# Kernel optimization log

Measured on AMD Instinct MI355X. Metric: run time of the kernel, lower is better.

## Reference

```python
import jax, jax.numpy as jnp
import numpy as np

N_NODES = 100_000
N_EDGES = 1_600_000
IN_F = 256
HID = 256
OUT_F = 256
BN_EPS = 1e-5


def make_quaternion_mul(kernel):
    # kernel: [d, 4m] -> hamilton: [4d, 4m]
    dim = kernel.shape[1] // 4
    r, i, j, k = jnp.split(kernel, 4, axis=1)
    r2 = jnp.concatenate([r, -i, -j, -k], axis=0)
    i2 = jnp.concatenate([i, r, -k, j], axis=0)
    j2 = jnp.concatenate([j, k, r, -i], axis=0)
    k2 = jnp.concatenate([k, -j, i, r], axis=0)
    return jnp.concatenate([r2, i2, j2, k2], axis=1)


def setup_inputs() -> dict:
    key = jax.random.key(0)
    ks = jax.random.split(key, 6)
    x = jax.random.normal(ks[0], (N_NODES, IN_F), dtype=jnp.float32)
    rows = jax.random.randint(ks[1], (N_EDGES,), 0, N_NODES, dtype=jnp.int32)
    cols = jax.random.randint(ks[2], (N_EDGES,), 0, N_NODES, dtype=jnp.int32)
    edge_vals = jax.random.uniform(ks[3], (N_EDGES,), dtype=jnp.float32)
    stdv1 = np.sqrt(6.0 / (IN_F // 4 + HID))
    weight1 = jax.random.uniform(ks[4], (IN_F // 4, HID), dtype=jnp.float32,
                                 minval=-stdv1, maxval=stdv1)
    stdv2 = np.sqrt(6.0 / (HID // 4 + OUT_F))
    weight2 = jax.random.uniform(ks[5], (HID // 4, OUT_F), dtype=jnp.float32,
                                 minval=-stdv2, maxval=stdv2)
    gamma = jnp.ones((HID,), dtype=jnp.float32)
    beta = jnp.zeros((HID,), dtype=jnp.float32)
    return {"x": x, "rows": rows, "cols": cols, "edge_vals": edge_vals,
            "weight1": weight1, "weight2": weight2, "gamma": gamma, "beta": beta}


def reference(x, rows, cols, edge_vals, weight1, weight2, gamma, beta):
    hamilton1 = make_quaternion_mul(weight1)  # [IN_F, HID]
    hamilton2 = make_quaternion_mul(weight2)  # [HID, OUT_F]
    # spmm: new_x[r] = sum_e adj[r,c]*x[c] over edges (r=rows, c=cols)
    gathered = edge_vals[:, None] * x[cols]               # [E, IN_F]
    new_x = jax.ops.segment_sum(gathered, rows, num_segments=N_NODES)
    out1 = new_x @ hamilton1                              # [N, HID]
    # BatchNorm1d (training mode): biased batch stats over nodes
    mean = jnp.mean(out1, axis=0)
    var = jnp.mean(jnp.square(out1 - mean), axis=0)
    out1 = (out1 - mean) * jax.lax.rsqrt(var + BN_EPS) * gamma + beta
    out1 = jnp.tanh(out1)
    return out1 @ hamilton2                               # [N, OUT_F]
```

## Files before the change

kernel.cpp:

```cpp
#include <hip/hip_runtime.h>
#include <hip/hip_bf16.h>
#include <math.h>


#define FDIM 256
#define NREP 32
#define CH 2048

typedef __attribute__((ext_vector_type(8))) short bf16x8;
typedef __attribute__((ext_vector_type(4))) float f32x4;

static __device__ inline short f2bf(float x) {
    __hip_bfloat16 h = __float2bfloat16(x);
    return *reinterpret_cast<short*>(&h);
}
static __device__ inline float bf2f(unsigned short u) {
    union { unsigned int i; float f; } c;
    c.i = ((unsigned int)u) << 16;
    return c.f;
}
static __device__ inline float bflo(unsigned int u) {
    union { unsigned int i; float f; } c;
    c.i = u << 16;
    return c.f;
}
static __device__ inline float bfhi(unsigned int u) {
    union { unsigned int i; float f; } c;
    c.i = u & 0xFFFF0000u;
    return c.f;
}
static __device__ inline float fast_tanh(float x) {
    float e = __expf(2.f * x);
    return 1.f - 2.f * __builtin_amdgcn_rcpf(e + 1.f);
}

static __device__ void build_hfrag(const float* __restrict__ w, ushort* __restrict__ hf,
                                   int t) {
    const int   comp_t[16] = {0,1,2,3,  1,0,3,2,  2,3,0,1,  3,2,1,0};
    const float sign_t[16] = {1,1,1,1, -1,1,1,-1, -1,-1,1,1, -1,1,-1,1};
    int f = t >> 6, lane = t & 63;
    int tile = f >> 3, kk = f & 7;
    int col = tile * 16 + (lane & 15);
    int b = col >> 6, q = col & 63;
    ushort o[8];
#pragma unroll
    for (int j = 0; j < 8; ++j) {
        int k = kk * 32 + ((lane >> 4) << 3) + j;
        int a = k >> 6, p = k & 63;
        int ab = a * 4 + b;
        float v = sign_t[ab] * w[p * 256 + comp_t[ab] * 64 + q];
        o[j] = (ushort)f2bf(v);
    }
    *(ushort4*)(hf + (size_t)t * 8)     = make_ushort4(o[0], o[1], o[2], o[3]);
    *(ushort4*)(hf + (size_t)t * 8 + 4) = make_ushort4(o[4], o[5], o[6], o[7]);
}

__global__ void k_init(const float* __restrict__ w1, const float* __restrict__ w2,
                       ushort* __restrict__ h1f, ushort* __restrict__ h2f,
                       float* __restrict__ statsR) {
    int b = blockIdx.x;
    if (b < 32) {
        build_hfrag(w1, h1f, b * 256 + threadIdx.x);
    } else if (b < 64) {
        build_hfrag(w2, h2f, (b - 32) * 256 + threadIdx.x);
    } else {
        int slot = (b - 64) * 256 + threadIdx.x;
        *(float4*)(statsR + slot * 4) = make_float4(0.f, 0.f, 0.f, 0.f);
    }
}

__global__ __launch_bounds__(256) void k_p1(const int* __restrict__ rows,
                                            int* __restrict__ CM,
                                            int E, int nchunk, int NB) {
    __shared__ int lc[256];
    int t = threadIdx.x, c = blockIdx.x;
    lc[t] = 0;
    __syncthreads();
#pragma unroll
    for (int i = 0; i < 8; ++i) {
        int e = c * CH + i * 256 + t;
        if (e < E) atomicAdd(&lc[rows[e] >> 9], 1);
    }
    __syncthreads();
    if (t < NB) CM[t * nchunk + c] = lc[t];
}

__global__ __launch_bounds__(256) void k_p2(const int* __restrict__ CM,
                                            int* __restrict__ PO,
                                            int* __restrict__ BT, int nchunk) {
    __shared__ int ts[256];
    int t = threadIdx.x, b = blockIdx.x;
    int base = b * nchunk;
    int lex[4], s = 0;
#pragma unroll
    for (int i = 0; i < 4; ++i) {
        int c = t * 4 + i;
        int v = (c < nchunk) ? CM[base + c] : 0;
        lex[i] = s;
        s += v;
    }
    ts[t] = s;
    __syncthreads();
    for (int off = 1; off < 256; off <<= 1) {
        int v = (t >= off) ? ts[t - off] : 0;
        __syncthreads();
        ts[t] += v;
        __syncthreads();
    }
    int excl = ts[t] - s;
#pragma unroll
    for (int i = 0; i < 4; ++i) {
        int c = t * 4 + i;
        if (c < nchunk) PO[base + c] = excl + lex[i];
    }
    if (t == 255) BT[b] = ts[255];
}

__global__ __launch_bounds__(256) void k_p3(const int* __restrict__ rows,
                                            const int* __restrict__ cols,
                                            const float* __restrict__ vals,
                                            const int* __restrict__ PO,
                                            const int* __restrict__ BT,
                                            uint2* __restrict__ tmp2,
                                            int E, int nchunk, int NB) {
    __shared__ int sBB[256];
    __shared__ int sPO[256];
    __shared__ int sLC[256];
    int t = threadIdx.x, c = blockIdx.x;
    int own = (t < NB) ? BT[t] : 0;
    sBB[t] = own;
    sPO[t] = (t < NB) ? PO[t * nchunk + c] : 0;
    sLC[t] = 0;
    __syncthreads();
    for (int off = 1; off < 256; off <<= 1) {
        int v = (t >= off) ? sBB[t - off] : 0;
        __syncthreads();
        sBB[t] += v;
        __syncthreads();
    }
    sBB[t] -= own;
    __syncthreads();
#pragma unroll
    for (int i = 0; i < 8; ++i) {
        int e = c * CH + i * 256 + t;
        if (e < E) {
            int r = rows[e];
            int b = r >> 9;
            int rank = atomicAdd(&sLC[b], 1);
            int pos = sBB[b] + sPO[b] + rank;
            int iv = (int)(vals[e] * 32768.0f);
            tmp2[pos] = make_uint2((unsigned int)cols[e] | ((unsigned int)iv << 17),
                                   (unsigned int)r);
        }
    }
}

__global__ __launch_bounds__(1024) void k_p4(const uint2* __restrict__ tmp2,
                                             const int* __restrict__ BT,
                                             unsigned int* __restrict__ ew,
                                             int* __restrict__ offs,
                                             int N, int NB) {
    __shared__ int sBB[256];
    __shared__ int sH[512];
    __shared__ int sO[512];
    __shared__ int sC[512];
    int t = threadIdx.x, b = blockIdx.x;
    int own = 0;
    if (t < 256) {
        own = (t < NB) ? BT[t] : 0;
        sBB[t] = own;
    }
    __syncthreads();
    for (int off = 1; off < 256; off <<= 1) {
        int v = (t < 256 && t >= off) ? sBB[t - off] : 0;
        __syncthreads();
        if (t < 256) sBB[t] += v;
        __syncthreads();
    }
    if (t < 256) sBB[t] -= own;
    if (t < 512) sH[t] = 0;
    __syncthreads();
    const int base = sBB[b];
    const int nE = BT[b];
    const int rbase = b << 9;
    for (int i = t; i < nE; i += 1024)
        atomicAdd(&sH[(int)tmp2[base + i].y - rbase], 1);
    __syncthreads();
    if (t < 512) sO[t] = sH[t];
    __syncthreads();
    for (int off = 1; off < 512; off <<= 1) {
        int v = (t < 512 && t >= off) ? sO[t - off] : 0;
        __syncthreads();
        if (t < 512) sO[t] += v;
        __syncthreads();
    }
    if (t < 512) {
        sO[t] -= sH[t];
        int r = rbase + t;
        if (r <= N) offs[r] = base + sO[t];
        sC[t] = 0;
    }
    __syncthreads();
    for (int i = t; i < nE; i += 1024) {
        uint2 u = tmp2[base + i];
        int lr = (int)u.y - rbase;
        int p = atomicAdd(&sC[lr], 1);
        ew[base + sO[lr] + p] = u.x;
    }
}

__global__ __launch_bounds__(256) void k_gemm1(const float* __restrict__ X,
                                               const ushort* __restrict__ Bf,
                                               ushort* __restrict__ Y, int N) {
    __shared__ ushort lds[16384];
    const int t = threadIdx.x;
    const int w = t >> 6, lane = t & 63;
    const int r0 = blockIdx.x * 128 + w * 32;
    const int kbase = ((lane >> 4) & 3) * 8;
    const int rA[2] = { min(r0 + (lane & 15), N - 1),
                        min(r0 + 16 + (lane & 15), N - 1) };

    bf16x8 af[2][8];
#pragma unroll
    for (int rt = 0; rt < 2; ++rt)
#pragma unroll
        for (int kk = 0; kk < 8; ++kk) {
            const float* p = X + (size_t)rA[rt] * 256 + kk * 32 + kbase;
            float4 v0 = *(const float4*)p;
            float4 v1 = *(const float4*)(p + 4);
            bf16x8 a;
            a[0] = f2bf(v0.x); a[1] = f2bf(v0.y); a[2] = f2bf(v0.z); a[3] = f2bf(v0.w);
            a[4] = f2bf(v1.x); a[5] = f2bf(v1.y); a[6] = f2bf(v1.z); a[7] = f2bf(v1.w);
            af[rt][kk] = a;
        }

    for (int g = 0; g < 4; ++g) {
        {
            const float4* s4 = (const float4*)(Bf + (size_t)g * 16384 + t * 64);
            float4* d4 = (float4*)(lds + t * 64);
#pragma unroll
            for (int i = 0; i < 8; ++i) d4[i] = s4[i];
        }
        __syncthreads();

        f32x4 acc[2][4];
#pragma unroll
        for (int rt = 0; rt < 2; ++rt)
#pragma unroll
            for (int tg = 0; tg < 4; ++tg) acc[rt][tg] = (f32x4){0.f, 0.f, 0.f, 0.f};

#pragma unroll
        for (int tg = 0; tg < 4; ++tg)
#pragma unroll
            for (int kk = 0; kk < 8; ++kk) {
                bf16x8 b = *(const bf16x8*)(lds + ((tg * 8 + kk) * 64 + lane) * 8);
                acc[0][tg] = __builtin_amdgcn_mfma_f32_16x16x32_bf16(af[0][kk], b, acc[0][tg], 0, 0, 0);
                acc[1][tg] = __builtin_amdgcn_mfma_f32_16x16x32_bf16(af[1][kk], b, acc[1][tg], 0, 0, 0);
            }

#pragma unroll
        for (int tg = 0; tg < 4; ++tg) {
            int col = (g * 4 + tg) * 16 + (lane & 15);
#pragma unroll
            for (int rt = 0; rt < 2; ++rt) {
                int rbase = r0 + rt * 16 + ((lane >> 4) & 3) * 4;
#pragma unroll
                for (int j = 0; j < 4; ++j) {
                    int r = rbase + j;
                    if (r < N) Y[(size_t)r * 256 + col] = (ushort)f2bf(acc[rt][tg][j]);
                }
            }
        }
        __syncthreads();
    }
}

__global__ __launch_bounds__(256) void k_spmm(const ushort* __restrict__ Y,
                                              const int* __restrict__ offs,
                                              const unsigned int* __restrict__ ew,
                                              ushort* __restrict__ O,
                                              float* __restrict__ statsR, int n) {
    __shared__ float ls[8][256];
    const int tid = threadIdx.x;
    int wid = (blockIdx.x * blockDim.x + tid) >> 6;
    int w = tid >> 6, lane = tid & 63;
    int l32 = lane & 31;
    int row = wid * 2 + (lane >> 5);
    bool ok = row < n;
    int r = ok ? row : 0;
    int beg = offs[r];
    int cnt = ok ? (offs[r + 1] - beg) : 0;
    int g = (cnt + 7) >> 3;
    const unsigned int* ep = ew + beg;

    float a0 = 0.f, a1 = 0.f, a2 = 0.f, a3 = 0.f;
    float a4 = 0.f, a5 = 0.f, a6 = 0.f, a7 = 0.f;

    for (int gi = 0; gi < g; ++gi) {
        unsigned int wv[8];
#pragma unroll
        for (int i = 0; i < 8; ++i) wv[i] = ep[gi * 8 + i];
        uint4 u[8];
#pragma unroll
        for (int i = 0; i < 8; ++i) {
            int c = (gi * 8 + i < cnt) ? (int)(wv[i] & 0x1FFFFu) : 0;
            u[i] = *(const uint4*)(Y + (size_t)c * 256 + l32 * 8);
        }
#pragma unroll
        for (int i = 0; i < 8; ++i) {
            float v = (gi * 8 + i < cnt) ? (float)(wv[i] >> 17) * (1.0f / 32768.0f) : 0.f;
            a0 = fmaf(v, bflo(u[i].x), a0); a1 = fmaf(v, bfhi(u[i].x), a1);
            a2 = fmaf(v, bflo(u[i].y), a2); a3 = fmaf(v, bfhi(u[i].y), a3);
            a4 = fmaf(v, bflo(u[i].z), a4); a5 = fmaf(v, bfhi(u[i].z), a5);
            a6 = fmaf(v, bflo(u[i].w), a6); a7 = fmaf(v, bfhi(u[i].w), a7);
        }
    }
    if (ok) {
        unsigned int p0 = ((unsigned int)(unsigned short)f2bf(a0)) |
                          (((unsigned int)(unsigned short)f2bf(a1)) << 16);
        unsigned int p1 = ((unsigned int)(unsigned short)f2bf(a2)) |
                          (((unsigned int)(unsigned short)f2bf(a3)) << 16);
        unsigned int p2 = ((unsigned int)(unsigned short)f2bf(a4)) |
                          (((unsigned int)(unsigned short)f2bf(a5)) << 16);
        unsigned int p3 = ((unsigned int)(unsigned short)f2bf(a6)) |
                          (((unsigned int)(unsigned short)f2bf(a7)) << 16);
        *(uint4*)(O + (size_t)r * 512 + l32 * 8) = make_uint4(p0, p1, p2, p3);
    }

    int h2 = w * 2 + (lane >> 5);
    int fb = l32 * 8;
    int rep = blockIdx.x & (NREP - 1);
    *(float4*)&ls[h2][fb]     = make_float4(a0, a1, a2, a3);
    *(float4*)&ls[h2][fb + 4] = make_float4(a4, a5, a6, a7);
    __syncthreads();
    float sv = 0.f;
#pragma unroll
    for (int i = 0; i < 8; ++i) sv += ls[i][tid];
    atomicAdd(&statsR[rep * 256 + tid], sv);
    __syncthreads();
    *(float4*)&ls[h2][fb]     = make_float4(a0 * a0, a1 * a1, a2 * a2, a3 * a3);
    *(float4*)&ls[h2][fb + 4] = make_float4(a4 * a4, a5 * a5, a6 * a6, a7 * a7);
    __syncthreads();
    float qv = 0.f;
#pragma unroll
    for (int i = 0; i < 8; ++i) qv += ls[i][tid];
    atomicAdd(&statsR[NREP * 256 + rep * 256 + tid], qv);
}

__global__ __launch_bounds__(256) void k_gemm2(void* __restrict__ Av,
                                               const ushort* __restrict__ Bf,
                                               const float* __restrict__ statsR,
                                               const float* __restrict__ gamma,
                                               const float* __restrict__ beta, int N) {
    __shared__ ushort lds[16384];
    __shared__ float sscl[256], sshf[256];
    const int t = threadIdx.x;
    const int w = t >> 6, lane = t & 63;
    const int r0 = blockIdx.x * 128 + w * 32;
    const int kbase = ((lane >> 4) & 3) * 8;
    const int rA[2] = { min(r0 + (lane & 15), N - 1),
                        min(r0 + 16 + (lane & 15), N - 1) };

    {
        float s = 0.f, q = 0.f;
#pragma unroll
        for (int i = 0; i < NREP; ++i) {
            s += statsR[i * 256 + t];
            q += statsR[NREP * 256 + i * 256 + t];
        }
        float invn = 1.0f / (float)N;
        float mean = s * invn;
        float var = q * invn - mean * mean;
        float inv = rsqrtf(var + 1e-5f);
        float gg = gamma[t] * inv;
        sscl[t] = gg;
        sshf[t] = beta[t] - mean * gg;
        __syncthreads();
    }

    const ushort* X = (const ushort*)Av;
    bf16x8 af[2][8];
#pragma unroll
    for (int rt = 0; rt < 2; ++rt)
#pragma unroll
        for (int kk = 0; kk < 8; ++kk) {
            const ushort* p = X + (size_t)rA[rt] * 512 + kk * 32 + kbase;
            ushort4 u0 = *(const ushort4*)p;
            ushort4 u1 = *(const ushort4*)(p + 4);
            float4 s0 = *(const float4*)&sscl[kk * 32 + kbase];
            float4 s1 = *(const float4*)&sscl[kk * 32 + kbase + 4];
            float4 h0 = *(const float4*)&sshf[kk * 32 + kbase];
            float4 h1 = *(const float4*)&sshf[kk * 32 + kbase + 4];
            bf16x8 a;
            a[0] = f2bf(fast_tanh(fmaf(bf2f(u0.x), s0.x, h0.x)));
            a[1] = f2bf(fast_tanh(fmaf(bf2f(u0.y), s0.y, h0.y)));
            a[2] = f2bf(fast_tanh(fmaf(bf2f(u0.z), s0.z, h0.z)));
            a[3] = f2bf(fast_tanh(fmaf(bf2f(u0.w), s0.w, h0.w)));
            a[4] = f2bf(fast_tanh(fmaf(bf2f(u1.x), s1.x, h1.x)));
            a[5] = f2bf(fast_tanh(fmaf(bf2f(u1.y), s1.y, h1.y)));
            a[6] = f2bf(fast_tanh(fmaf(bf2f(u1.z), s1.z, h1.z)));
            a[7] = f2bf(fast_tanh(fmaf(bf2f(u1.w), s1.w, h1.w)));
            af[rt][kk] = a;
        }

    float* Cf = (float*)Av;
    for (int g = 0; g < 4; ++g) {
        {
            const float4* s4 = (const float4*)(Bf + (size_t)g * 16384 + t * 64);
            float4* d4 = (float4*)(lds + t * 64);
#pragma unroll
            for (int i = 0; i < 8; ++i) d4[i] = s4[i];
        }
        __syncthreads();

        f32x4 acc[2][4];
#pragma unroll
        for (int rt = 0; rt < 2; ++rt)
#pragma unroll
            for (int tg = 0; tg < 4; ++tg) acc[rt][tg] = (f32x4){0.f, 0.f, 0.f, 0.f};

#pragma unroll
        for (int tg = 0; tg < 4; ++tg)
#pragma unroll
            for (int kk = 0; kk < 8; ++kk) {
                bf16x8 b = *(const bf16x8*)(lds + ((tg * 8 + kk) * 64 + lane) * 8);
                acc[0][tg] = __builtin_amdgcn_mfma_f32_16x16x32_bf16(af[0][kk], b, acc[0][tg], 0, 0, 0);
                acc[1][tg] = __builtin_amdgcn_mfma_f32_16x16x32_bf16(af[1][kk], b, acc[1][tg], 0, 0, 0);
            }

#pragma unroll
        for (int tg = 0; tg < 4; ++tg) {
            int col = (g * 4 + tg) * 16 + (lane & 15);
#pragma unroll
            for (int rt = 0; rt < 2; ++rt) {
                int rbase = r0 + rt * 16 + ((lane >> 4) & 3) * 4;
#pragma unroll
                for (int j = 0; j < 4; ++j) {
                    int r = rbase + j;
                    if (r < N) Cf[(size_t)r * 256 + col] = acc[rt][tg][j];
                }
            }
        }
        __syncthreads();
    }
}

extern "C" void kernel_launch(void* const* d_in, const int* in_sizes, int n_in,
                              void* d_out, int out_size, void* d_ws, size_t ws_size,
                              hipStream_t stream) {
    const float* x     = (const float*)d_in[0];
    const int* rows    = (const int*)d_in[1];
    const int* cols    = (const int*)d_in[2];
    const float* evin  = (const float*)d_in[3];
    const float* w1    = (const float*)d_in[4];
    const float* w2    = (const float*)d_in[5];
    const float* gamma = (const float*)d_in[6];
    const float* beta  = (const float*)d_in[7];
    float* out = (float*)d_out;

    const int N = in_sizes[0] / FDIM;
    const int E = in_sizes[1];
    const int NB = (N + 511) >> 9;
    const int nchunk = (E + CH - 1) / CH;

    char* ws = (char*)d_ws;
    size_t o = 0;
    auto alloc = [&](size_t bytes) -> char* {
        char* p = ws + o;
        o += (bytes + 255) & ~(size_t)255;
        return p;
    };
    ushort* h1f  = (ushort*)alloc(128 * 64 * 8 * 2);
    ushort* h2f  = (ushort*)alloc(128 * 64 * 8 * 2);
    ushort* y    = (ushort*)alloc((size_t)N * 256 * 2);
    float* statsR = (float*)alloc(2 * NREP * 256 * 4);
    int*   CM    = (int*)alloc((size_t)NB * nchunk * 4);
    int*   PO    = (int*)alloc((size_t)NB * nchunk * 4);
    int*   BT    = (int*)alloc(256 * 4);
    uint2* tmp2  = (uint2*)alloc((size_t)E * 8);
    unsigned int* ewp = (unsigned int*)alloc(((size_t)E + 8) * 4);
    int*   offs  = (int*)alloc((size_t)(N + 1) * 4);

    k_init<<<80, 256, 0, stream>>>(w1, w2, h1f, h2f, statsR);
    k_p1<<<nchunk, 256, 0, stream>>>(rows, CM, E, nchunk, NB);
    k_p2<<<NB, 256, 0, stream>>>(CM, PO, BT, nchunk);
    k_p3<<<nchunk, 256, 0, stream>>>(rows, cols, evin, PO, BT, tmp2, E, nchunk, NB);
    k_p4<<<NB, 1024, 0, stream>>>(tmp2, BT, ewp, offs, N, NB);

    int gblk = (N + 127) / 128;
    k_gemm1<<<gblk, 256, 0, stream>>>(x, h1f, y, N);
    k_spmm<<<(N + 7) / 8, 256, 0, stream>>>(y, offs, ewp, (ushort*)out, statsR, N);
    k_gemm2<<<gblk, 256, 0, stream>>>(out, h2f, statsR, gamma, beta, N);
}
```

Baseline: 295.0 us.

## Prefetch GEMM weight tiles into registers and remap SpMM to one row per wave

Both GEMM kernels now load the next weight group into registers while the current group computes, hiding global-load latency behind the MFMA work. The SpMM kernel assigns one full wave per row (4 features per lane, 8-byte loads) instead of a half-wave per row, and software-prefetches the next batch of packed edge words. This doubles the SpMM grid size and the number of stats atomics, adds register pressure in the GEMMs, and enlarges the edge buffer padding to cover the prefetch reads.

After: 353.8 us. 1.2x slower.

```diff
diff --git a/kernel.cpp b/kernel.cpp
--- a/kernel.cpp
+++ b/kernel.cpp
@@ -234,14 +234,24 @@
             af[rt][kk] = a;
         }
 
+    float4 breg[8];
+#pragma unroll
+    for (int i = 0; i < 8; ++i)
+        breg[i] = ((const float4*)(Bf + (size_t)0 * 16384 + t * 64))[i];
+
+#pragma unroll
     for (int g = 0; g < 4; ++g) {
         {
-            const float4* s4 = (const float4*)(Bf + (size_t)g * 16384 + t * 64);
             float4* d4 = (float4*)(lds + t * 64);
 #pragma unroll
-            for (int i = 0; i < 8; ++i) d4[i] = s4[i];
-        }
-        __syncthreads();
+            for (int i = 0; i < 8; ++i) d4[i] = breg[i];
+        }
+        __syncthreads();
+        if (g < 3) {
+            const float4* s4 = (const float4*)(Bf + (size_t)(g + 1) * 16384 + t * 64);
+#pragma unroll
+            for (int i = 0; i < 8; ++i) breg[i] = s4[i];
+        }
 
         f32x4 acc[2][4];
 #pragma unroll
@@ -280,70 +290,63 @@
                                               const unsigned int* __restrict__ ew,
                                               ushort* __restrict__ O,
                                               float* __restrict__ statsR, int n) {
-    __shared__ float ls[8][256];
+    __shared__ float ls[4][256];
     const int tid = threadIdx.x;
-    int wid = (blockIdx.x * blockDim.x + tid) >> 6;
-    int w = tid >> 6, lane = tid & 63;
-    int l32 = lane & 31;
-    int row = wid * 2 + (lane >> 5);
+    const int w = tid >> 6, lane = tid & 63;
+    int row = blockIdx.x * 4 + w;
     bool ok = row < n;
     int r = ok ? row : 0;
     int beg = offs[r];
-    int cnt = ok ? (offs[r + 1] - beg) : 0;
+    int cnt = ok ? offs[r + 1] - beg : 0;
     int g = (cnt + 7) >> 3;
     const unsigned int* ep = ew + beg;
 
     float a0 = 0.f, a1 = 0.f, a2 = 0.f, a3 = 0.f;
-    float a4 = 0.f, a5 = 0.f, a6 = 0.f, a7 = 0.f;
-
+
+    unsigned int wv[8];
+    if (g > 0) {
+#pragma unroll
+        for (int i = 0; i < 8; ++i) wv[i] = ep[i];
+    }
     for (int gi = 0; gi < g; ++gi) {
-        unsigned int wv[8];
-#pragma unroll
-        for (int i = 0; i < 8; ++i) wv[i] = ep[gi * 8 + i];
-        uint4 u[8];
+        unsigned int wn[8];
+        bool more = (gi + 1) < g;
+        if (more) {
+#pragma unroll
+            for (int i = 0; i < 8; ++i) wn[i] = ep[(gi + 1) * 8 + i];
+        }
 #pragma unroll
         for (int i = 0; i < 8; ++i) {
-            int c = (gi * 8 + i < cnt) ? (int)(wv[i] & 0x1FFFFu) : 0;
-            u[i] = *(const uint4*)(Y + (size_t)c * 256 + l32 * 8);
-        }
-#pragma unroll
-        for (int i = 0; i < 8; ++i) {
-            float v = (gi * 8 + i < cnt) ? (float)(wv[i] >> 17) * (1.0f / 32768.0f) : 0.f;
-            a0 = fmaf(v, bflo(u[i].x), a0); a1 = fmaf(v, bfhi(u[i].x), a1);
-            a2 = fmaf(v, bflo(u[i].y), a2); a3 = fmaf(v, bfhi(u[i].y), a3);
-            a4 = fmaf(v, bflo(u[i].z), a4); a5 = fmaf(v, bfhi(u[i].z), a5);
-            a6 = fmaf(v, bflo(u[i].w), a6); a7 = fmaf(v, bfhi(u[i].w), a7);
+            int idx = gi * 8 + i;
+            unsigned int wd = wv[i];
+            int c = (idx < cnt) ? (int)(wd & 0x1FFFFu) : 0;
+            float v = (idx < cnt) ? (float)(wd >> 17) * (1.0f / 32768.0f) : 0.f;
+            ushort4 yv = *(const ushort4*)(Y + (size_t)c * 256 + lane * 4);
+            a0 = fmaf(v, bf2f(yv.x), a0);
+            a1 = fmaf(v, bf2f(yv.y), a1);
+            a2 = fmaf(v, bf2f(yv.z), a2);
+            a3 = fmaf(v, bf2f(yv.w), a3);
+        }
+        if (more) {
+#pragma unroll
+            for (int i = 0; i < 8; ++i) wv[i] = wn[i];
         }
     }
     if (ok) {
-        unsigned int p0 = ((unsigned int)(unsigned short)f2bf(a0)) |
-                          (((unsigned int)(unsigned short)f2bf(a1)) << 16);
-        unsigned int p1 = ((unsigned int)(unsigned short)f2bf(a2)) |
-                          (((unsigned int)(unsigned short)f2bf(a3)) << 16);
-        unsigned int p2 = ((unsigned int)(unsigned short)f2bf(a4)) |
-                          (((unsigned int)(unsigned short)f2bf(a5)) << 16);
-        unsigned int p3 = ((unsigned int)(unsigned short)f2bf(a6)) |
-                          (((unsigned int)(unsigned short)f2bf(a7)) << 16);
-        *(uint4*)(O + (size_t)r * 512 + l32 * 8) = make_uint4(p0, p1, p2, p3);
-    }
-
-    int h2 = w * 2 + (lane >> 5);
-    int fb = l32 * 8;
+        ushort4 o = make_ushort4((ushort)f2bf(a0), (ushort)f2bf(a1),
+                                 (ushort)f2bf(a2), (ushort)f2bf(a3));
+        *(ushort4*)(O + (size_t)r * 512 + lane * 4) = o;
+    }
+
     int rep = blockIdx.x & (NREP - 1);
-    *(float4*)&ls[h2][fb]     = make_float4(a0, a1, a2, a3);
-    *(float4*)&ls[h2][fb + 4] = make_float4(a4, a5, a6, a7);
-    __syncthreads();
-    float sv = 0.f;
-#pragma unroll
-    for (int i = 0; i < 8; ++i) sv += ls[i][tid];
+    *(float4*)&ls[w][lane * 4] = make_float4(a0, a1, a2, a3);
+    __syncthreads();
+    float sv = ls[0][tid] + ls[1][tid] + ls[2][tid] + ls[3][tid];
     atomicAdd(&statsR[rep * 256 + tid], sv);
     __syncthreads();
-    *(float4*)&ls[h2][fb]     = make_float4(a0 * a0, a1 * a1, a2 * a2, a3 * a3);
-    *(float4*)&ls[h2][fb + 4] = make_float4(a4 * a4, a5 * a5, a6 * a6, a7 * a7);
-    __syncthreads();
-    float qv = 0.f;
-#pragma unroll
-    for (int i = 0; i < 8; ++i) qv += ls[i][tid];
+    *(float4*)&ls[w][lane * 4] = make_float4(a0 * a0, a1 * a1, a2 * a2, a3 * a3);
+    __syncthreads();
+    float qv = ls[0][tid] + ls[1][tid] + ls[2][tid] + ls[3][tid];
     atomicAdd(&statsR[NREP * 256 + rep * 256 + tid], qv);
 }
 
@@ -403,15 +406,25 @@
             af[rt][kk] = a;
         }
 
+    float4 breg[8];
+#pragma unroll
+    for (int i = 0; i < 8; ++i)
+        breg[i] = ((const float4*)(Bf + (size_t)0 * 16384 + t * 64))[i];
+
     float* Cf = (float*)Av;
+#pragma unroll
     for (int g = 0; g < 4; ++g) {
         {
-            const float4* s4 = (const float4*)(Bf + (size_t)g * 16384 + t * 64);
             float4* d4 = (float4*)(lds + t * 64);
 #pragma unroll
-            for (int i = 0; i < 8; ++i) d4[i] = s4[i];
-        }
-        __syncthreads();
+            for (int i = 0; i < 8; ++i) d4[i] = breg[i];
+        }
+        __syncthreads();
+        if (g < 3) {
+            const float4* s4 = (const float4*)(Bf + (size_t)(g + 1) * 16384 + t * 64);
+#pragma unroll
+            for (int i = 0; i < 8; ++i) breg[i] = s4[i];
+        }
 
         f32x4 acc[2][4];
 #pragma unroll
@@ -478,7 +491,7 @@
     int*   PO    = (int*)alloc((size_t)NB * nchunk * 4);
     int*   BT    = (int*)alloc(256 * 4);
     uint2* tmp2  = (uint2*)alloc((size_t)E * 8);
-    unsigned int* ewp = (unsigned int*)alloc(((size_t)E + 8) * 4);
+    unsigned int* ewp = (unsigned int*)alloc(((size_t)E + 16) * 4);
     int*   offs  = (int*)alloc((size_t)(N + 1) * 4);
 
     k_init<<<80, 256, 0, stream>>>(w1, w2, h1f, h2f, statsR);
@@ -489,6 +502,6 @@
 
     int gblk = (N + 127) / 128;
     k_gemm1<<<gblk, 256, 0, stream>>>(x, h1f, y, N);
-    k_spmm<<<(N + 7) / 8, 256, 0, stream>>>(y, offs, ewp, (ushort*)out, statsR, N);
+    k_spmm<<<(N + 3) / 4, 256, 0, stream>>>(y, offs, ewp, (ushort*)out, statsR, N);
     k_gemm2<<<gblk, 256, 0, stream>>>(out, h2f, statsR, gamma, beta, N);
 }
```
